# Performance work log

Hardware: AMD Instinct MI355X
Metric: run time of the kernel (lower is better)

The kernel has to match this reference:

```python
import jax, jax.numpy as jnp
import numpy as np

N_PATHS = 10_000_000
MAX_LEN = 3
N_NODES = 100_000
HIDDEN = 128
HEAD = 1


def setup_inputs() -> dict:
    key = jax.random.key(0)
    k1, k2, k3 = jax.random.split(key, 3)
    # path indices in [-1, N_NODES); -1 marks a padding slot (maps to zero score)
    paths = jax.random.randint(k1, (N_PATHS, MAX_LEN), -1, N_NODES, dtype=jnp.int64)
    node_feature = jax.random.normal(k2, (N_NODES, HIDDEN), dtype=jnp.float32)
    # per-step Linear(hidden, head=1, bias=False) weights, stacked: [MAX_LEN, HEAD, HIDDEN]
    W = jax.random.normal(k3, (MAX_LEN, HEAD, HIDDEN), dtype=jnp.float32) * (1.0 / np.sqrt(HIDDEN))
    return {"paths": paths, "node_feature": node_feature, "W": W}


def reference(paths, node_feature, W):
    # per-step scalar node scores: [n_nodes, L, head]
    proj = jnp.einsum("nd,lod->nlo", node_feature, W)
    valid = paths >= 0                         # [P, L]
    safe = jnp.where(valid, paths, 0)          # clamp -1 -> 0 (masked below)
    L = W.shape[0]
    step = jnp.arange(L)[None, :]              # [1, L]
    gathered = proj[safe, step, :]             # [P, L, head]
    gathered = jnp.where(valid[..., None], gathered, jnp.zeros((), proj.dtype))
    path_length = jnp.clip(valid.sum(axis=-1, keepdims=True), 1)  # [P, 1]
    attn_score = gathered.sum(axis=1) / path_length.astype(proj.dtype)  # [P, head]
    return attn_score
```

## Files before the change

kernel.cpp:

```cpp
#include <hip/hip_runtime.h>

#define HIDDEN   128
#define TPB      1024
#define PPT      12
#define CN       38400
#define CN2      76800
#define DUMMY2   (2 * CN2)
#define UNITS    (CN2 / 1024)

typedef unsigned short u16;
typedef unsigned int   u32;

static __device__ __forceinline__ u16 f32_to_f16_bits(float x) {
    union { _Float16 h; u16 u; } cv;
    cv.h = (_Float16)x;
    return cv.u;
}

static __device__ __forceinline__ void gload_lds16(const void* gp, void* lp) {
    __builtin_amdgcn_global_load_lds(
        (const __attribute__((address_space(1))) unsigned int*)gp,
        (__attribute__((address_space(3))) unsigned int*)lp,
        16, 0, 0);
}

__global__ __launch_bounds__(256) void proj_kernel(
    const float* __restrict__ feat,
    const float* __restrict__ W,
    u16* __restrict__ proj_h,
    int n_nodes)
{
    int gtid = blockIdx.x * blockDim.x + threadIdx.x;
    int node = gtid >> 6;
    int lane = threadIdx.x & 63;
    if (node >= n_nodes) return;

    const float2* f2 = (const float2*)(feat + (size_t)node * HIDDEN);
    const float2* w2 = (const float2*)W;

    float2 f   = f2[lane];
    float2 w0  = w2[lane];
    float2 w1  = w2[64 + lane];
    float2 wv2 = w2[128 + lane];

    float s0 = f.x * w0.x  + f.y * w0.y;
    float s1 = f.x * w1.x  + f.y * w1.y;
    float s2 = f.x * wv2.x + f.y * wv2.y;

    #pragma unroll
    for (int off = 32; off > 0; off >>= 1) {
        s0 += __shfl_xor(s0, off, 64);
        s1 += __shfl_xor(s1, off, 64);
        s2 += __shfl_xor(s2, off, 64);
    }

    if (lane == 0) {
        u16* base = proj_h + node;
        base[0]                   = f32_to_f16_bits(s0);
        base[n_nodes]             = f32_to_f16_bits(s1);
        base[2 * (size_t)n_nodes] = f32_to_f16_bits(s2);
    }
}

__global__ __launch_bounds__(TPB, 4) void score_kernel(
    const int* __restrict__ paths,
    const u16* __restrict__ proj_h,
    float* __restrict__ out,
    int n_paths, int n_nodes, int nh)
{
    extern __shared__ u16 lds[];
    char* ldsb = (char*)lds;

    int base = blockIdx.x * (TPB * PPT) + threadIdx.x;
    int wid  = threadIdx.x >> 6;
    int lane = threadIdx.x & 63;

    const unsigned char* tab = (const unsigned char*)proj_h;
    int plane_b = 2 * n_nodes;
    int NC      = 3 * nh;

    {
        int units0 = plane_b >= CN2 ? UNITS : ((plane_b + 1023) >> 10);
        for (int j = wid; j < units0; j += TPB / 64)
            gload_lds16(tab + (size_t)j * 1024 + lane * 16,
                        ldsb + j * 1024);
    }
    if (threadIdx.x == 0) lds[DUMMY2 / 2] = 0;

    int id2[3 * PPT];
    #pragma unroll
    for (int k = 0; k < PPT; ++k) {
        int idx = base + k * TPB;
        int ii  = idx < n_paths ? idx : (n_paths - 1);
        const int* pp = paths + (size_t)ii * 3;
        id2[3*k+0] = __builtin_nontemporal_load(pp + 0) << 1;
        id2[3*k+1] = __builtin_nontemporal_load(pp + 1) << 1;
        id2[3*k+2] = __builtin_nontemporal_load(pp + 2) << 1;
    }

    float acc[PPT];
    #pragma unroll
    for (int k = 0; k < PPT; ++k) acc[k] = 0.0f;

    __syncthreads();

    for (int h = 0; h < nh; ++h) {
        #pragma unroll
        for (int l = 0; l < 3; ++l) {
            int c = h * 3 + l;

            if (c + 1 < NC) {
                int       hn    = (l == 2) ? (h + 1) : h;
                const int ln    = (l == 2) ? 0 : (l + 1);
                int       nbase = ((c + 1) & 1) * CN2;
                const unsigned char* src = tab + (size_t)ln * plane_b
                                               + (size_t)hn * CN2;
                int rem_b = plane_b - hn * CN2;
                int units = rem_b >= CN2 ? UNITS : ((rem_b + 1023) >> 10);
                for (int j = wid; j < units; j += TPB / 64)
                    gload_lds16(src + (size_t)j * 1024 + lane * 16,
                                ldsb + nbase + j * 1024);
            }

            int cb2 = h * CN2;
            int bb  = (c & 1) * CN2;
            #pragma unroll
            for (int k = 0; k < PPT; ++k) {
                u32 loc2 = (u32)(id2[3*k + l] - cb2);
                int off  = loc2 < (u32)CN2 ? (bb + (int)loc2) : DUMMY2;
                union { u16 u; _Float16 hh; } cv;
                cv.u = *(const u16*)(ldsb + off);
                acc[k] += (float)cv.hh;
            }

            if (c + 1 < NC) __syncthreads();
        }
    }

    #pragma unroll
    for (int k = 0; k < PPT; ++k) {
        int idx = base + k * TPB;
        if (idx < n_paths) {
            int cnt = (int)(id2[3*k] >= 0) + (int)(id2[3*k+1] >= 0)
                    + (int)(id2[3*k+2] >= 0);
            float inv = (cnt == 3) ? (1.0f/3.0f) : (cnt == 2 ? 0.5f : 1.0f);
            __builtin_nontemporal_store(acc[k] * inv, out + idx);
        }
    }
}

extern "C" void kernel_launch(void* const* d_in, const int* in_sizes, int n_in,
                              void* d_out, int out_size, void* d_ws, size_t ws_size,
                              hipStream_t stream) {
    const int*   paths = (const int*)d_in[0];
    const float* feat  = (const float*)d_in[1];
    const float* W     = (const float*)d_in[2];
    float*       out   = (float*)d_out;

    int n_nodes = in_sizes[1] / HIDDEN;
    int n_paths = in_sizes[0] / 3;
    u16* proj_h = (u16*)d_ws;

    int nh = (n_nodes + CN - 1) / CN;
    size_t lds_bytes = (size_t)2 * CN2 + 4;

    (void)hipFuncSetAttribute((const void*)score_kernel,
            hipFuncAttributeMaxDynamicSharedMemorySize, (int)lds_bytes);
    (void)hipGetLastError();

    {
        int blocks = (n_nodes + 3) / 4;
        proj_kernel<<<blocks, 256, 0, stream>>>(feat, W, proj_h, n_nodes);
    }

    {
        int blocks = (n_paths + TPB * PPT - 1) / (TPB * PPT);
        score_kernel<<<blocks, TPB, lds_bytes, stream>>>(paths, proj_h, out,
                                                         n_paths, n_nodes, nh);
    }
}
```

Baseline: 254.3 us.

## Raise paths per thread and add fully unrolled three-chunk score kernel

Raises paths per thread from 12 to 20, so each block's nine LDS table-chunk loads serve more paths and fewer blocks reload the table. Adds a specialised kernel for the three-chunk case whose chunk loop is fully unrolled with constant offsets. Moves the second buffer to a padded offset with a per-buffer zero slot and sets waves-per-EU via an attribute. The cost is more registers per thread (60 ids plus 20 accumulators) and fewer blocks overall, which could leave part of the GPU idle at the tail.

```diff
diff --git a/kernel.cpp b/kernel.cpp
--- a/kernel.cpp
+++ b/kernel.cpp
@@ -1,12 +1,14 @@
 #include <hip/hip_runtime.h>
 
-#define HIDDEN   128
-#define TPB      1024
-#define PPT      12
-#define CN       38400
-#define CN2      76800
-#define DUMMY2   (2 * CN2)
-#define UNITS    (CN2 / 1024)
+#define HIDDEN    128
+#define TPB       1024
+#define PPT       20
+#define CN        38400
+#define CN2       76800
+#define BUF1      76816
+#define ZERO_GAP  76800
+#define LDS_BYTES 153620
+#define UNITS     (CN2 / 1024)
 
 typedef unsigned short u16;
 typedef unsigned int   u32;
@@ -62,11 +64,13 @@
     }
 }
 
-__global__ __launch_bounds__(TPB, 4) void score_kernel(
+__global__ __launch_bounds__(TPB)
+__attribute__((amdgpu_waves_per_eu(4, 4)))
+void score_kernel(
     const int* __restrict__ paths,
     const u16* __restrict__ proj_h,
     float* __restrict__ out,
-    int n_paths, int n_nodes, int nh)
+    int n_paths, int n_nodes)
 {
     extern __shared__ u16 lds[];
     char* ldsb = (char*)lds;
@@ -77,15 +81,14 @@
 
     const unsigned char* tab = (const unsigned char*)proj_h;
     int plane_b = 2 * n_nodes;
-    int NC      = 3 * nh;
-
-    {
-        int units0 = plane_b >= CN2 ? UNITS : ((plane_b + 1023) >> 10);
-        for (int j = wid; j < units0; j += TPB / 64)
-            gload_lds16(tab + (size_t)j * 1024 + lane * 16,
-                        ldsb + j * 1024);
-    }
-    if (threadIdx.x == 0) lds[DUMMY2 / 2] = 0;
+
+    for (int j = wid; j < UNITS; j += TPB / 64)
+        gload_lds16(tab + (size_t)j * 1024 + lane * 16, ldsb + j * 1024);
+
+    if (threadIdx.x == 0) {
+        *(u32*)(ldsb + ZERO_GAP)        = 0;
+        *(u32*)(ldsb + BUF1 + ZERO_GAP) = 0;
+    }
 
     int id2[3 * PPT];
     #pragma unroll
@@ -104,35 +107,120 @@
 
     __syncthreads();
 
+    #pragma unroll
+    for (int c = 0; c < 9; ++c) {
+        const int h   = c / 3;
+        const int l   = c - 3 * h;
+        const int cb2 = h * CN2;
+        const int bb  = (c & 1) ? BUF1 : 0;
+
+        if (c + 1 < 9) {
+            const int hn   = (c + 1) / 3;
+            const int ln   = (c + 1) - 3 * hn;
+            const int nb   = ((c + 1) & 1) ? BUF1 : 0;
+            const int ncb2 = hn * CN2;
+            int rem   = plane_b - ncb2;
+            int units = rem >= CN2 ? UNITS : ((rem + 1023) >> 10);
+            const unsigned char* src = tab + (size_t)ln * plane_b + ncb2;
+            for (int j = wid; j < units; j += TPB / 64)
+                gload_lds16(src + (size_t)j * 1024 + lane * 16,
+                            ldsb + nb + j * 1024);
+        }
+
+        #pragma unroll
+        for (int k = 0; k < PPT; ++k) {
+            u32 loc2 = (u32)(id2[3*k + l] - cb2);
+            u32 off  = loc2 < (u32)CN2 ? loc2 : (u32)CN2;
+            union { u16 u; _Float16 hh; } cv;
+            cv.u = *(const u16*)(ldsb + bb + off);
+            acc[k] += (float)cv.hh;
+        }
+
+        if (c + 1 < 9) __syncthreads();
+    }
+
+    #pragma unroll
+    for (int k = 0; k < PPT; ++k) {
+        int idx = base + k * TPB;
+        if (idx < n_paths) {
+            int cnt = (int)(id2[3*k] >= 0) + (int)(id2[3*k+1] >= 0)
+                    + (int)(id2[3*k+2] >= 0);
+            float inv = (cnt == 3) ? (1.0f/3.0f) : (cnt == 2 ? 0.5f : 1.0f);
+            __builtin_nontemporal_store(acc[k] * inv, out + idx);
+        }
+    }
+}
+
+__global__ __launch_bounds__(TPB)
+__attribute__((amdgpu_waves_per_eu(4, 4)))
+void score_generic(
+    const int* __restrict__ paths, const u16* __restrict__ proj_h,
+    float* __restrict__ out, int n_paths, int n_nodes, int nh)
+{
+    extern __shared__ u16 lds[];
+    char* ldsb = (char*)lds;
+
+    int base = blockIdx.x * (TPB * PPT) + threadIdx.x;
+    int wid  = threadIdx.x >> 6;
+    int lane = threadIdx.x & 63;
+
+    const unsigned char* tab = (const unsigned char*)proj_h;
+    int plane_b = 2 * n_nodes;
+    int NC      = 3 * nh;
+
+    {
+        int units0 = plane_b >= CN2 ? UNITS : ((plane_b + 1023) >> 10);
+        for (int j = wid; j < units0; j += TPB / 64)
+            gload_lds16(tab + (size_t)j * 1024 + lane * 16, ldsb + j * 1024);
+    }
+    if (threadIdx.x == 0) {
+        *(u32*)(ldsb + ZERO_GAP)        = 0;
+        *(u32*)(ldsb + BUF1 + ZERO_GAP) = 0;
+    }
+
+    int id2[3 * PPT];
+    #pragma unroll
+    for (int k = 0; k < PPT; ++k) {
+        int idx = base + k * TPB;
+        int ii  = idx < n_paths ? idx : (n_paths - 1);
+        const int* pp = paths + (size_t)ii * 3;
+        id2[3*k+0] = __builtin_nontemporal_load(pp + 0) << 1;
+        id2[3*k+1] = __builtin_nontemporal_load(pp + 1) << 1;
+        id2[3*k+2] = __builtin_nontemporal_load(pp + 2) << 1;
+    }
+
+    float acc[PPT];
+    #pragma unroll
+    for (int k = 0; k < PPT; ++k) acc[k] = 0.0f;
+
+    __syncthreads();
+
     for (int h = 0; h < nh; ++h) {
         #pragma unroll
         for (int l = 0; l < 3; ++l) {
             int c = h * 3 + l;
-
             if (c + 1 < NC) {
-                int       hn    = (l == 2) ? (h + 1) : h;
-                const int ln    = (l == 2) ? 0 : (l + 1);
-                int       nbase = ((c + 1) & 1) * CN2;
+                int       hn = (l == 2) ? (h + 1) : h;
+                const int ln = (l == 2) ? 0 : (l + 1);
+                int       nb = ((c + 1) & 1) ? BUF1 : 0;
                 const unsigned char* src = tab + (size_t)ln * plane_b
                                                + (size_t)hn * CN2;
-                int rem_b = plane_b - hn * CN2;
-                int units = rem_b >= CN2 ? UNITS : ((rem_b + 1023) >> 10);
+                int rem   = plane_b - hn * CN2;
+                int units = rem >= CN2 ? UNITS : ((rem + 1023) >> 10);
                 for (int j = wid; j < units; j += TPB / 64)
                     gload_lds16(src + (size_t)j * 1024 + lane * 16,
-                                ldsb + nbase + j * 1024);
+                                ldsb + nb + j * 1024);
             }
-
             int cb2 = h * CN2;
-            int bb  = (c & 1) * CN2;
+            int bb  = (c & 1) ? BUF1 : 0;
             #pragma unroll
             for (int k = 0; k < PPT; ++k) {
                 u32 loc2 = (u32)(id2[3*k + l] - cb2);
-                int off  = loc2 < (u32)CN2 ? (bb + (int)loc2) : DUMMY2;
+                u32 off  = loc2 < (u32)CN2 ? loc2 : (u32)CN2;
                 union { u16 u; _Float16 hh; } cv;
-                cv.u = *(const u16*)(ldsb + off);
+                cv.u = *(const u16*)(ldsb + bb + off);
                 acc[k] += (float)cv.hh;
             }
-
             if (c + 1 < NC) __syncthreads();
         }
     }
@@ -162,10 +250,8 @@
     u16* proj_h = (u16*)d_ws;
 
     int nh = (n_nodes + CN - 1) / CN;
-    size_t lds_bytes = (size_t)2 * CN2 + 4;
-
-    (void)hipFuncSetAttribute((const void*)score_kernel,
-            hipFuncAttributeMaxDynamicSharedMemorySize, (int)lds_bytes);
+    size_t lds_bytes = LDS_BYTES;
+
     (void)hipGetLastError();
 
     {
@@ -175,7 +261,16 @@
 
     {
         int blocks = (n_paths + TPB * PPT - 1) / (TPB * PPT);
-        score_kernel<<<blocks, TPB, lds_bytes, stream>>>(paths, proj_h, out,
-                                                         n_paths, n_nodes, nh);
-    }
-}
+        if (nh == 3) {
+            (void)hipFuncSetAttribute((const void*)score_kernel,
+                    hipFuncAttributeMaxDynamicSharedMemorySize, (int)lds_bytes);
+            score_kernel<<<blocks, TPB, lds_bytes, stream>>>(
+                paths, proj_h, out, n_paths, n_nodes);
+        } else {
+            (void)hipFuncSetAttribute((const void*)score_generic,
+                    hipFuncAttributeMaxDynamicSharedMemorySize, (int)lds_bytes);
+            score_generic<<<blocks, TPB, lds_bytes, stream>>>(
+                paths, proj_h, out, n_paths, n_nodes, nh);
+        }
+    }
+}
```

New measurement: 289.2 us. 1.14x slower.
